# Kernel optimization log

Hardware: AMD Instinct MI355X
Metric: run time of the kernel (lower is better)

## Reference

```python
import jax, jax.numpy as jnp
import numpy as np

B, C_IN, C_OUT, RED, H, W = 8, 256, 64, 16, 256, 256
K = 3


def setup_inputs() -> dict:
    key = jax.random.key(0)
    k1, k2, k3, k4, k5 = jax.random.split(key, 5)
    x = jax.random.normal(k1, (B, C_OUT, H, W), dtype=jnp.float32)
    vec = jax.random.normal(k2, (B, C_IN), dtype=jnp.float32)
    # ChanNorm affine params
    g = jnp.ones((1, C_OUT, 1, 1), dtype=jnp.float32)
    b = jnp.zeros((1, C_OUT, 1, 1), dtype=jnp.float32)
    # conv_du MLP (torch Linear weights: [out, in], no bias)
    w1 = jax.random.normal(k3, (C_IN // RED, C_IN), dtype=jnp.float32) / np.sqrt(C_IN)
    w2 = jax.random.normal(k4, (C_OUT, C_IN // RED), dtype=jnp.float32) / np.sqrt(C_IN // RED)
    # Conv2DMod weight, kaiming normal fan_in (leaky_relu a=0): std=sqrt(2/fan_in)
    fan_in = C_OUT * K * K
    wconv = jax.random.normal(k5, (C_OUT, C_OUT, K, K), dtype=jnp.float32) * np.sqrt(2.0 / fan_in)
    return {"x": x, "vec": vec, "g": g, "b": b, "w1": w1, "w2": w2, "wconv": wconv}


def reference(x, vec, g, b, w1, w2, wconv):
    eps_norm = 1e-5
    eps_mod = 1e-8
    # ChanNorm: normalize over channel dim (unbiased=False var)
    mean = jnp.mean(x, axis=1, keepdims=True)
    var = jnp.mean((x - mean) ** 2, axis=1, keepdims=True)
    nx = (x - mean) / jnp.sqrt(var + eps_norm) * g + b
    # style MLP: Linear -> LeakyReLU(0.1) -> Linear (no biases)
    hid = jax.nn.leaky_relu(vec @ w1.T, negative_slope=0.1)
    sty = hid @ w2.T  # [B, C_OUT]
    # per-sample modulated weights: [B, O, I, K, K]
    weights = wconv[None, :, :, :, :] * (sty[:, None, :, None, None] + 1.0)
    # demodulate
    d = jax.lax.rsqrt(jnp.sum(weights ** 2, axis=(2, 3, 4), keepdims=True) + eps_mod)
    weights = weights * d
    # grouped conv with groups=B == per-sample conv; same padding for k=3,s=1,d=1 -> 1
    pad = ((H - 1) * 0 + 1 * (K - 1)) // 2
    def per_sample_conv(xi, wi):
        # xi: [C,H,W], wi: [O,I,K,K]
        return jax.lax.conv_general_dilated(
            xi[None], wi, window_strides=(1, 1),
            padding=[(pad, pad), (pad, pad)],
            dimension_numbers=("NCHW", "OIHW", "NCHW"))[0]
    out = jax.vmap(per_sample_conv)(nx, weights)  # [B, O, H, W]
    return out + x
```

## Files before the change

### kernel.cpp

```cpp
#include <hip/hip_runtime.h>
#include <hip/hip_bf16.h>

typedef __hip_bfloat16 bf16;
typedef __attribute__((ext_vector_type(8))) short short8;
typedef __attribute__((ext_vector_type(4))) float float4v;

#define Hd 256
#define Wd 256
#define HW 65536
#define CO 64

__global__ __launch_bounds__(64) void k1_style(
    const float* __restrict__ vec, const float* __restrict__ w1,
    const float* __restrict__ w2, const float* __restrict__ wconv,
    bf16* __restrict__ wA)
{
    int o = blockIdx.x;
    int s = blockIdx.y;
    int i = threadIdx.x;

    float sv[4];
#pragma unroll
    for (int q = 0; q < 4; ++q) sv[q] = vec[s * 256 + q * 64 + i];

    float hid[16];
#pragma unroll
    for (int j = 0; j < 16; ++j) {
        float p = 0.f;
#pragma unroll
        for (int q = 0; q < 4; ++q) p += sv[q] * w1[j * 256 + q * 64 + i];
#pragma unroll
        for (int off = 32; off >= 1; off >>= 1) p += __shfl_xor(p, off, 64);
        hid[j] = p > 0.f ? p : 0.1f * p;
    }
    float sty = 0.f;
#pragma unroll
    for (int j = 0; j < 16; ++j) sty += w2[i * 16 + j] * hid[j];
    float msty = sty + 1.0f;

    float wrow[9];
#pragma unroll
    for (int tt = 0; tt < 9; ++tt) wrow[tt] = wconv[(o * 64 + i) * 9 + tt] * msty;
    float ss = 0.f;
#pragma unroll
    for (int tt = 0; tt < 9; ++tt) ss += wrow[tt] * wrow[tt];
#pragma unroll
    for (int off = 32; off >= 1; off >>= 1) ss += __shfl_xor(ss, off, 64);
    float d = rsqrtf(ss + 1e-8f);

    bf16* wAs = wA + s * (18 * 64 * 32);
#pragma unroll
    for (int tt = 0; tt < 9; ++tt) {
        int k = tt * 64 + i;
        wAs[(k >> 5) * 2048 + o * 32 + (k & 31)] = (bf16)(wrow[tt] * d);
    }
}

__global__ __launch_bounds__(256) void k2_norm(
    const float* __restrict__ x, const float* __restrict__ gg,
    const float* __restrict__ bb, bf16* __restrict__ nx,
    float2* __restrict__ sms)
{
    int h = blockIdx.x, s = blockIdx.y;
    int t = threadIdx.x;
    int cg = t & 15;
    int pg = t >> 4;
    float4 g4 = *(const float4*)&gg[cg * 4];
    float4 b4 = *(const float4*)&bb[cg * 4];
    const float* xrow = x + (size_t)s * ((size_t)CO * HW) + (size_t)h * Wd;
    bf16*   nxrow  = nx  + ((size_t)s * HW + (size_t)h * Wd) * CO;
    float2* smsrow = sms +  (size_t)s * HW + (size_t)h * Wd;

#pragma unroll 1
    for (int it = 0; it < 4; ++it) {
        int px = it * 64 + pg * 4;
        float4 v[4];
#pragma unroll
        for (int cc = 0; cc < 4; ++cc)
            v[cc] = *(const float4*)&xrow[(size_t)(cg * 4 + cc) * HW + px];

        float s1[4], s2[4];
#pragma unroll
        for (int pi = 0; pi < 4; ++pi) {
            float a0 = (&v[0].x)[pi], a1 = (&v[1].x)[pi];
            float a2 = (&v[2].x)[pi], a3 = (&v[3].x)[pi];
            s1[pi] = (a0 + a1) + (a2 + a3);
            s2[pi] = (a0 * a0 + a1 * a1) + (a2 * a2 + a3 * a3);
        }
#pragma unroll
        for (int off = 1; off <= 8; off <<= 1)
#pragma unroll
            for (int pi = 0; pi < 4; ++pi) {
                s1[pi] += __shfl_xor(s1[pi], off, 64);
                s2[pi] += __shfl_xor(s2[pi], off, 64);
            }
        float mean[4], rstd[4], stdv[4];
#pragma unroll
        for (int pi = 0; pi < 4; ++pi) {
            mean[pi] = s1[pi] * (1.f / 64);
            float var = s2[pi] * (1.f / 64) - mean[pi] * mean[pi];
            rstd[pi] = rsqrtf(var + 1e-5f);
            stdv[pi] = sqrtf(var + 1e-5f);
        }
        if (cg == 0) {
#pragma unroll
            for (int pi = 0; pi < 4; ++pi)
                smsrow[px + pi] = make_float2(mean[pi], stdv[pi]);
        }
#pragma unroll
        for (int pi = 0; pi < 4; ++pi) {
            union { uint2 u; bf16 hh[4]; } o;
#pragma unroll
            for (int cc = 0; cc < 4; ++cc) {
                float f  = (&v[cc].x)[pi];
                float gv = (&g4.x)[cc], bv = (&b4.x)[cc];
                o.hh[cc] = (bf16)((f - mean[pi]) * rstd[pi] * gv + bv);
            }
            *(uint2*)&nxrow[(size_t)(px + pi) * CO + cg * 4] = o.u;
        }
    }
}

#define PXB 32
#define ROWS 8
#define TR 10
#define WL 34
#define NSITES (TR * WL)
#define ROW_ELEMS (8 * WL * 8)

union U4 { uint4 u; bf16 h[8]; short8 s8; };

__global__ __launch_bounds__(256) void k3_conv(
    const bf16* __restrict__ nx, const float2* __restrict__ sms,
    const float* __restrict__ gg, const float* __restrict__ bb,
    const bf16* __restrict__ wA, float* __restrict__ out)
{
    int w0 = blockIdx.x * PXB;
    int h0 = blockIdx.y * ROWS;
    int s  = blockIdx.z;
    int t  = threadIdx.x;
    __shared__ __align__(16) bf16 tile[TR * ROW_ELEMS];
    __shared__ float2 sbi[64];
    if (t < 64) sbi[t] = make_float2(bb[t], 1.0f / gg[t]);

    int p0 = t, p1 = t + 256;
    bool live1 = (p1 < NSITES);
    int dr0 = p0 / WL, wl0 = p0 - dr0 * WL;
    int dr1 = live1 ? (p1 / WL) : 0;
    int wl1 = live1 ? (p1 - dr1 * WL) : 0;
    int grow0 = h0 + dr0 - 1, wab0 = w0 + wl0 - 1;
    int grow1 = h0 + dr1 - 1, wab1 = w0 + wl1 - 1;
    bool ok0 = (grow0 >= 0 && grow0 < Hd && wab0 >= 0 && wab0 < Wd);
    bool ok1 = live1 && (grow1 >= 0 && grow1 < Hd && wab1 >= 0 && wab1 < Wd);
    const bf16* np0 = nx + ((size_t)s * HW + (size_t)grow0 * Wd + wab0) * CO;
    const bf16* np1 = nx + ((size_t)s * HW + (size_t)grow1 * Wd + wab1) * CO;
    bf16* dst0 = &tile[dr0 * ROW_ELEMS + wl0 * 8];
    bf16* dst1 = &tile[dr1 * ROW_ELEMS + wl1 * 8];
    uint4 z = make_uint4(0u, 0u, 0u, 0u);
#pragma unroll
    for (int c8 = 0; c8 < 8; ++c8) {
        uint4 a = ok0 ? *(const uint4*)&np0[c8 * 8] : z;
        *(uint4*)&dst0[c8 * (WL * 8)] = a;
    }
    if (live1) {
#pragma unroll
        for (int c8 = 0; c8 < 8; ++c8) {
            uint4 a = ok1 ? *(const uint4*)&np1[c8 * 8] : z;
            *(uint4*)&dst1[c8 * (WL * 8)] = a;
        }
    }

    int wave = t >> 6, lane = t & 63;
    int mi = wave & 1, ni = wave >> 1;
    int col = lane & 15, quad = lane >> 4;

    const bf16* wAs = wA + s * (18 * 64 * 32);
    short8 afrag[18][2];
#pragma unroll
    for (int kc = 0; kc < 18; ++kc)
#pragma unroll
        for (int mt = 0; mt < 2; ++mt) {
            U4 a;
            a.u = *(const uint4*)&wAs[kc * 2048 + (mi * 32 + mt * 16 + col) * 32 + quad * 8];
            afrag[kc][mt] = a.s8;
        }
    int wpx = w0 + ni * 16 + col;
    float2 msr[ROWS];
#pragma unroll
    for (int r = 0; r < ROWS; ++r)
        msr[r] = sms[(size_t)s * HW + (size_t)(h0 + r) * Wd + wpx];

    __syncthreads();

    int wl_i = ni * 16 + col + 1;
#pragma unroll 2
    for (int r = 0; r < ROWS; ++r) {
        float4v acc[2];
        acc[0] = (float4v)0.f; acc[1] = (float4v)0.f;
#pragma unroll
        for (int kc = 0; kc < 18; ++kc) {
            int tap = kc >> 1;
            int kh = tap / 3, kw = tap - kh * 3;
            int ch8 = (kc & 1) * 4 + quad;
            U4 b;
            b.u = *(const uint4*)&tile[(r + kh) * ROW_ELEMS + (ch8 * WL + ni * 16 + col + kw) * 8];
            acc[0] = __builtin_amdgcn_mfma_f32_16x16x32_bf16(afrag[kc][0], b.s8, acc[0], 0, 0, 0);
            acc[1] = __builtin_amdgcn_mfma_f32_16x16x32_bf16(afrag[kc][1], b.s8, acc[1], 0, 0, 0);
        }
        int grow = h0 + r;
        float2 ms = msr[r];
#pragma unroll
        for (int mt = 0; mt < 2; ++mt) {
#pragma unroll
            for (int rr = 0; rr < 4; ++rr) {
                int o = mi * 32 + mt * 16 + quad * 4 + rr;
                float nxf = __bfloat162float(
                    tile[(r + 1) * ROW_ELEMS + ((o >> 3) * WL + wl_i) * 8 + (o & 7)]);
                float2 bi = sbi[o];
                float xrec = (nxf - bi.x) * bi.y * ms.y + ms.x;
                size_t idx = (size_t)(s * CO + o) * HW + (size_t)grow * Wd + wpx;
                out[idx] = acc[mt][rr] + xrec;
            }
        }
    }
}

extern "C" void kernel_launch(void* const* d_in, const int* in_sizes, int n_in,
                              void* d_out, int out_size, void* d_ws, size_t ws_size,
                              hipStream_t stream)
{
    const float* x     = (const float*)d_in[0];
    const float* vec   = (const float*)d_in[1];
    const float* g     = (const float*)d_in[2];
    const float* bb    = (const float*)d_in[3];
    const float* w1    = (const float*)d_in[4];
    const float* w2    = (const float*)d_in[5];
    const float* wconv = (const float*)d_in[6];
    float* out = (float*)d_out;

    char* wsb = (char*)d_ws;
    bf16*   wA  = (bf16*)wsb;
    bf16*   nx  = (bf16*)(wsb + ((size_t)1 << 20));
    float2* sms = (float2*)(wsb + ((size_t)65 << 20));

    k1_style<<<dim3(64, 8), 64, 0, stream>>>(vec, w1, w2, wconv, wA);
    k2_norm<<<dim3(256, 8), 256, 0, stream>>>(x, g, bb, nx, sms);
    k3_conv<<<dim3(8, 32, 8), 256, 0, stream>>>(nx, sms, g, bb, wA, out);
}
```

Before: 320.9 us.

## Reorder conv loop to stream weight fragments and split norm rows across blocks

The conv kernel now iterates over the K chunks in the outer loop and keeps accumulators for all 8 rows. Weight fragments are streamed from global memory one step ahead instead of preloading all 36 into registers. This lowers register pressure and exposes more independent MFMAs, at the cost of more live accumulators and per-step global loads. The norm kernel is split into quarter-row blocks with four times as many blocks, to increase parallelism.

```diff
diff --git a/kernel.cpp b/kernel.cpp
--- a/kernel.cpp
+++ b/kernel.cpp
@@ -61,63 +61,61 @@
     const float* __restrict__ bb, bf16* __restrict__ nx,
     float2* __restrict__ sms)
 {
-    int h = blockIdx.x, s = blockIdx.y;
-    int t = threadIdx.x;
+    int bx = blockIdx.x;
+    int h  = bx >> 2, qx = (bx & 3) * 64;
+    int s  = blockIdx.y;
+    int t  = threadIdx.x;
     int cg = t & 15;
     int pg = t >> 4;
+    int px = qx + pg * 4;
     float4 g4 = *(const float4*)&gg[cg * 4];
     float4 b4 = *(const float4*)&bb[cg * 4];
     const float* xrow = x + (size_t)s * ((size_t)CO * HW) + (size_t)h * Wd;
     bf16*   nxrow  = nx  + ((size_t)s * HW + (size_t)h * Wd) * CO;
     float2* smsrow = sms +  (size_t)s * HW + (size_t)h * Wd;
 
-#pragma unroll 1
-    for (int it = 0; it < 4; ++it) {
-        int px = it * 64 + pg * 4;
-        float4 v[4];
-#pragma unroll
-        for (int cc = 0; cc < 4; ++cc)
-            v[cc] = *(const float4*)&xrow[(size_t)(cg * 4 + cc) * HW + px];
-
-        float s1[4], s2[4];
+    float4 v[4];
+#pragma unroll
+    for (int cc = 0; cc < 4; ++cc)
+        v[cc] = *(const float4*)&xrow[(size_t)(cg * 4 + cc) * HW + px];
+
+    float s1[4], s2[4];
+#pragma unroll
+    for (int pi = 0; pi < 4; ++pi) {
+        float a0 = (&v[0].x)[pi], a1 = (&v[1].x)[pi];
+        float a2 = (&v[2].x)[pi], a3 = (&v[3].x)[pi];
+        s1[pi] = (a0 + a1) + (a2 + a3);
+        s2[pi] = (a0 * a0 + a1 * a1) + (a2 * a2 + a3 * a3);
+    }
+#pragma unroll
+    for (int off = 1; off <= 8; off <<= 1)
 #pragma unroll
         for (int pi = 0; pi < 4; ++pi) {
-            float a0 = (&v[0].x)[pi], a1 = (&v[1].x)[pi];
-            float a2 = (&v[2].x)[pi], a3 = (&v[3].x)[pi];
-            s1[pi] = (a0 + a1) + (a2 + a3);
-            s2[pi] = (a0 * a0 + a1 * a1) + (a2 * a2 + a3 * a3);
-        }
-#pragma unroll
-        for (int off = 1; off <= 8; off <<= 1)
-#pragma unroll
-            for (int pi = 0; pi < 4; ++pi) {
-                s1[pi] += __shfl_xor(s1[pi], off, 64);
-                s2[pi] += __shfl_xor(s2[pi], off, 64);
-            }
-        float mean[4], rstd[4], stdv[4];
-#pragma unroll
-        for (int pi = 0; pi < 4; ++pi) {
-            mean[pi] = s1[pi] * (1.f / 64);
-            float var = s2[pi] * (1.f / 64) - mean[pi] * mean[pi];
-            rstd[pi] = rsqrtf(var + 1e-5f);
-            stdv[pi] = sqrtf(var + 1e-5f);
-        }
-        if (cg == 0) {
-#pragma unroll
-            for (int pi = 0; pi < 4; ++pi)
-                smsrow[px + pi] = make_float2(mean[pi], stdv[pi]);
-        }
-#pragma unroll
-        for (int pi = 0; pi < 4; ++pi) {
-            union { uint2 u; bf16 hh[4]; } o;
-#pragma unroll
-            for (int cc = 0; cc < 4; ++cc) {
-                float f  = (&v[cc].x)[pi];
-                float gv = (&g4.x)[cc], bv = (&b4.x)[cc];
-                o.hh[cc] = (bf16)((f - mean[pi]) * rstd[pi] * gv + bv);
-            }
-            *(uint2*)&nxrow[(size_t)(px + pi) * CO + cg * 4] = o.u;
-        }
+            s1[pi] += __shfl_xor(s1[pi], off, 64);
+            s2[pi] += __shfl_xor(s2[pi], off, 64);
+        }
+    float mean[4], rstd[4];
+#pragma unroll
+    for (int pi = 0; pi < 4; ++pi) {
+        mean[pi] = s1[pi] * (1.f / 64);
+        float var = s2[pi] * (1.f / 64) - mean[pi] * mean[pi];
+        rstd[pi] = rsqrtf(var + 1e-5f);
+    }
+    if (cg == 0) {
+#pragma unroll
+        for (int pi = 0; pi < 4; ++pi)
+            smsrow[px + pi] = make_float2(mean[pi], sqrtf(s2[pi] * (1.f / 64) - mean[pi] * mean[pi] + 1e-5f));
+    }
+#pragma unroll
+    for (int pi = 0; pi < 4; ++pi) {
+        union { uint2 u; bf16 hh[4]; } o;
+#pragma unroll
+        for (int cc = 0; cc < 4; ++cc) {
+            float f  = (&v[cc].x)[pi];
+            float gv = (&g4.x)[cc], bv = (&b4.x)[cc];
+            o.hh[cc] = (bf16)((f - mean[pi]) * rstd[pi] * gv + bv);
+        }
+        *(uint2*)&nxrow[(size_t)(px + pi) * CO + cg * 4] = o.u;
     }
 }
 
@@ -175,15 +173,12 @@
     int col = lane & 15, quad = lane >> 4;
 
     const bf16* wAs = wA + s * (18 * 64 * 32);
-    short8 afrag[18][2];
-#pragma unroll
-    for (int kc = 0; kc < 18; ++kc)
-#pragma unroll
-        for (int mt = 0; mt < 2; ++mt) {
-            U4 a;
-            a.u = *(const uint4*)&wAs[kc * 2048 + (mi * 32 + mt * 16 + col) * 32 + quad * 8];
-            afrag[kc][mt] = a.s8;
-        }
+    const bf16* pa0 = wAs + (mi * 32 + col) * 32 + quad * 8;
+    const bf16* pa1 = wAs + (mi * 32 + 16 + col) * 32 + quad * 8;
+    U4 a0c, a1c;
+    a0c.u = *(const uint4*)pa0;
+    a1c.u = *(const uint4*)pa1;
+
     int wpx = w0 + ni * 16 + col;
     float2 msr[ROWS];
 #pragma unroll
@@ -192,21 +187,35 @@
 
     __syncthreads();
 
-    int wl_i = ni * 16 + col + 1;
-#pragma unroll 2
+    float4v acc[2][ROWS];
+#pragma unroll
+    for (int mt = 0; mt < 2; ++mt)
+#pragma unroll
+        for (int r = 0; r < ROWS; ++r) acc[mt][r] = (float4v)0.f;
+
+    int base = ni * 16 + col;
+#pragma unroll 1
+    for (int kc = 0; kc < 18; ++kc) {
+        U4 a0n, a1n;
+        a0n.u = *(const uint4*)(pa0 + (kc + 1) * 2048);
+        a1n.u = *(const uint4*)(pa1 + (kc + 1) * 2048);
+        int tap = kc >> 1;
+        int kh = (tap * 11) >> 5;
+        int kw = tap - kh * 3;
+        int ch8 = (kc & 1) * 4 + quad;
+        const bf16* bp = &tile[kh * ROW_ELEMS + (ch8 * WL + base + kw) * 8];
+#pragma unroll
+        for (int r = 0; r < ROWS; ++r) {
+            U4 b; b.u = *(const uint4*)&bp[r * ROW_ELEMS];
+            acc[0][r] = __builtin_amdgcn_mfma_f32_16x16x32_bf16(a0c.s8, b.s8, acc[0][r], 0, 0, 0);
+            acc[1][r] = __builtin_amdgcn_mfma_f32_16x16x32_bf16(a1c.s8, b.s8, acc[1][r], 0, 0, 0);
+        }
+        a0c = a0n; a1c = a1n;
+    }
+
+    int wl_i = base + 1;
+#pragma unroll
     for (int r = 0; r < ROWS; ++r) {
-        float4v acc[2];
-        acc[0] = (float4v)0.f; acc[1] = (float4v)0.f;
-#pragma unroll
-        for (int kc = 0; kc < 18; ++kc) {
-            int tap = kc >> 1;
-            int kh = tap / 3, kw = tap - kh * 3;
-            int ch8 = (kc & 1) * 4 + quad;
-            U4 b;
-            b.u = *(const uint4*)&tile[(r + kh) * ROW_ELEMS + (ch8 * WL + ni * 16 + col + kw) * 8];
-            acc[0] = __builtin_amdgcn_mfma_f32_16x16x32_bf16(afrag[kc][0], b.s8, acc[0], 0, 0, 0);
-            acc[1] = __builtin_amdgcn_mfma_f32_16x16x32_bf16(afrag[kc][1], b.s8, acc[1], 0, 0, 0);
-        }
         int grow = h0 + r;
         float2 ms = msr[r];
 #pragma unroll
@@ -219,7 +228,7 @@
                 float2 bi = sbi[o];
                 float xrec = (nxf - bi.x) * bi.y * ms.y + ms.x;
                 size_t idx = (size_t)(s * CO + o) * HW + (size_t)grow * Wd + wpx;
-                out[idx] = acc[mt][rr] + xrec;
+                out[idx] = acc[mt][r][rr] + xrec;
             }
         }
     }
@@ -244,6 +253,6 @@
     float2* sms = (float2*)(wsb + ((size_t)65 << 20));
 
     k1_style<<<dim3(64, 8), 64, 0, stream>>>(vec, w1, w2, wconv, wA);
-    k2_norm<<<dim3(256, 8), 256, 0, stream>>>(x, g, bb, nx, sms);
+    k2_norm<<<dim3(1024, 8), 256, 0, stream>>>(x, g, bb, nx, sms);
     k3_conv<<<dim3(8, 32, 8), 256, 0, stream>>>(nx, sms, g, bb, wA, out);
 }
```

New measurement: 324.9 us. About the same (+1.2%).
